# Kernel optimization log

Measured on AMD Instinct MI355X. Metric: run time of the kernel, lower is better.

Reference implementation:

```python
import jax, jax.numpy as jnp
import numpy as np

NEG_SLOPE = 0.2  # PyG GATConv default negative_slope


def gat_conv(x, src, dst, W, a_src, a_dst, bias, concat=True):
    """PyG-style GATConv (self-loops already appended to src/dst).
    x: [N, Fin], W: [Fin, H*C], a_src/a_dst: [H, C], bias: [H*C] or [C].
    """
    N = x.shape[0]
    H, C = a_src.shape
    h = (x @ W).reshape(N, H, C)                       # [N, H, C]
    s_src = jnp.einsum('nhc,hc->nh', h, a_src)         # per-node src logit
    s_dst = jnp.einsum('nhc,hc->nh', h, a_dst)         # per-node dst logit
    e = jax.nn.leaky_relu(s_src[src] + s_dst[dst], NEG_SLOPE)   # [E, H]
    # segment softmax over incoming edges of each destination node
    m = jax.ops.segment_max(e, dst, num_segments=N)    # [N, H]
    ex = jnp.exp(e - m[dst])
    denom = jax.ops.segment_sum(ex, dst, num_segments=N)
    alpha = ex / (denom[dst] + 1e-16)                  # [E, H]
    out = jax.ops.segment_sum(h[src] * alpha[:, :, None], dst, num_segments=N)  # [N,H,C]
    out = out.reshape(N, H * C) if concat else out.mean(axis=1)
    return out + bias


def setup_inputs() -> dict:
    key = jax.random.key(0)
    ks = jax.random.split(key, 12)
    N, E = 20000, 320000
    Fin, Hd, Hh = 384, 256, 4
    x = jax.random.normal(ks[0], (N, Fin), dtype=jnp.float32)
    edge_index = jax.random.randint(ks[1], (2, E), 0, N, dtype=jnp.int32)
    s = lambda k, shp, fan: jax.random.normal(k, shp, dtype=jnp.float32) / np.sqrt(fan)
    return {
        'x': x, 'edge_index': edge_index,
        'W1': s(ks[2], (Fin, Hh * Hd), Fin),
        'a_src1': s(ks[3], (Hh, Hd), Hd), 'a_dst1': s(ks[4], (Hh, Hd), Hd),
        'b1': jnp.zeros((Hh * Hd,), jnp.float32),
        'W2': s(ks[5], (Hh * Hd, Hd), Hh * Hd),
        'a_src2': s(ks[6], (1, Hd), Hd), 'a_dst2': s(ks[7], (1, Hd), Hd),
        'b2': jnp.zeros((Hd,), jnp.float32),
        'Wp1': s(ks[8], (Hd, Hd // 2), Hd), 'bp1': jnp.zeros((Hd // 2,), jnp.float32),
        'Wp2': s(ks[9], (Hd // 2, 1), Hd // 2), 'bp2': jnp.zeros((1,), jnp.float32),
    }


def reference(x, edge_index, W1, a_src1, a_dst1, b1, W2, a_src2, a_dst2, b2,
              Wp1, bp1, Wp2, bp2):
    N = x.shape[0]
    loops = jnp.arange(N, dtype=edge_index.dtype)
    src = jnp.concatenate([edge_index[0], loops])  # PyG add_self_loops=True
    dst = jnp.concatenate([edge_index[1], loops])
    h = jax.nn.elu(gat_conv(x, src, dst, W1, a_src1, a_dst1, b1, concat=True))
    h = jax.nn.elu(gat_conv(h, src, dst, W2, a_src2, a_dst2, b2, concat=True))
    graph_features = jnp.mean(h, axis=0, keepdims=True)  # batch=None path
    infl = jax.nn.sigmoid(jax.nn.relu(h @ Wp1 + bp1) @ Wp2 + bp2)
    return h, graph_features, infl
```

## Files before the change

### kernel.cpp

```cpp
#include <hip/hip_runtime.h>

#define NEG_SLOPE 0.2f
#define SM_SHIFT 3.0f

typedef __bf16 bf16x8 __attribute__((ext_vector_type(8)));
typedef float floatx4 __attribute__((ext_vector_type(4)));
typedef float floatx2 __attribute__((ext_vector_type(2)));
typedef unsigned short ushortx4 __attribute__((ext_vector_type(4)));
typedef unsigned short ushortx8 __attribute__((ext_vector_type(8)));

__device__ __forceinline__ float eluf(float x) { return x > 0.f ? x : __expf(x) - 1.f; }
__device__ __forceinline__ float lrelu(float x) { return x > 0.f ? x : NEG_SLOPE * x; }

__device__ __forceinline__ unsigned short f2bf(float f) {
    unsigned u = __float_as_uint(f);
    u += 0x7FFFu + ((u >> 16) & 1u);
    return (unsigned short)(u >> 16);
}
__device__ __forceinline__ float bf2f(unsigned short h) {
    return __uint_as_float(((unsigned)h) << 16);
}
__device__ __forceinline__ floatx2 mk2(unsigned u) {
    floatx2 r;
    r.x = __uint_as_float(u << 16);
    r.y = __uint_as_float(u & 0xFFFF0000u);
    return r;
}

__device__ __forceinline__ void async16(const unsigned short* g, unsigned short* l) {
    __builtin_amdgcn_global_load_lds(
        (const __attribute__((address_space(1))) unsigned int*)g,
        (__attribute__((address_space(3))) unsigned int*)l,
        16, 0, 0);
}

__global__ __launch_bounds__(256) void prep_kernel(
        const int* __restrict__ ei, int E, int N, int* __restrict__ counts,
        const float* __restrict__ x, unsigned short* __restrict__ xb,
        const float* __restrict__ W1, unsigned short* __restrict__ w1t,
        const float* __restrict__ W2, unsigned short* __restrict__ w2t,
        const float* __restrict__ Wp1, unsigned short* __restrict__ wp1t,
        const float* __restrict__ as1, const float* __restrict__ ad1, float* __restrict__ U) {
    __shared__ float tile[32][33];
    int b = blockIdx.x;
    int t = threadIdx.x;
    int Et = E + N;
    int nA = (Et + 255) >> 8;
    int nB = (N * 96 + 255) >> 8;
    if (b < nA) {
        int i = b * 256 + t;
        if (i < Et) {
            int d = (i < E) ? ei[E + i] : (i - E);
            atomicAdd(&counts[d], 1);
        }
    } else if (b < nA + nB) {
        int i = (b - nA) * 256 + t;
        if (i < N * 96) {
            float4 v = ((const float4*)x)[i];
            ushortx4 o;
            o[0] = f2bf(v.x); o[1] = f2bf(v.y); o[2] = f2bf(v.z); o[3] = f2bf(v.w);
            *(ushortx4*)(xb + (size_t)i * 4) = o;
        }
    } else if (b < nA + nB + 384) {
        int idx = b - nA - nB;
        int n0 = (idx & 31) * 32, k0 = (idx >> 5) * 32;
        int tx = t & 31, ty = t >> 5;
        #pragma unroll
        for (int i = 0; i < 32; i += 8)
            tile[ty + i][tx] = W1[(size_t)(k0 + ty + i) * 1024 + n0 + tx];
        __syncthreads();
        #pragma unroll
        for (int i = 0; i < 32; i += 8)
            w1t[(size_t)(n0 + ty + i) * 384 + k0 + tx] = f2bf(tile[tx][ty + i]);
    } else if (b < nA + nB + 384 + 256) {
        int idx = b - nA - nB - 384;
        int n0 = (idx & 7) * 32, k0 = (idx >> 3) * 32;
        int tx = t & 31, ty = t >> 5;
        #pragma unroll
        for (int i = 0; i < 32; i += 8)
            tile[ty + i][tx] = W2[(size_t)(k0 + ty + i) * 256 + n0 + tx];
        __syncthreads();
        #pragma unroll
        for (int i = 0; i < 32; i += 8)
            w2t[(size_t)(n0 + ty + i) * 1024 + k0 + tx] = f2bf(tile[tx][ty + i]);
    } else if (b < nA + nB + 384 + 256 + 32) {
        int idx = b - nA - nB - 384 - 256;
        int n0 = (idx & 3) * 32, k0 = (idx >> 2) * 32;
        int tx = t & 31, ty = t >> 5;
        #pragma unroll
        for (int i = 0; i < 32; i += 8)
            tile[ty + i][tx] = Wp1[(size_t)(k0 + ty + i) * 128 + n0 + tx];
        __syncthreads();
        #pragma unroll
        for (int i = 0; i < 32; i += 8)
            wp1t[(size_t)(n0 + ty + i) * 256 + k0 + tx] = f2bf(tile[tx][ty + i]);
    } else {
        int idx = b - nA - nB - 384 - 256 - 32;
        int k = idx * 4 + (t >> 6);
        int lane = t & 63;
        #pragma unroll
        for (int r = 0; r < 8; r++) {
            int h = r & 3;
            const float* a = (r < 4 ? as1 : ad1) + h * 256 + lane * 4;
            const float* w = W1 + (size_t)k * 1024 + h * 256 + lane * 4;
            float4 wv = *(const float4*)w;
            float4 av = *(const float4*)a;
            float p = wv.x * av.x + wv.y * av.y + wv.z * av.z + wv.w * av.w;
            #pragma unroll
            for (int off = 32; off; off >>= 1) p += __shfl_xor(p, off);
            if (lane == 0) U[r * 384 + k] = p;
        }
    }
}

__global__ void scan_kernel(int* __restrict__ counts_cursor, int* __restrict__ row_ptr, int N) {
    __shared__ int s_wsum[16];
    __shared__ int s_carry;
    int t = threadIdx.x;
    int lane = t & 63, wid = t >> 6;
    if (t == 0) { s_carry = 0; row_ptr[0] = 0; }
    __syncthreads();
    for (int start = 0; start < N; start += 1024) {
        int i = start + t;
        int v = (i < N) ? counts_cursor[i] : 0;
        int s = v;
        #pragma unroll
        for (int d = 1; d < 64; d <<= 1) {
            int u = __shfl_up(s, d);
            if (lane >= d) s += u;
        }
        if (lane == 63) s_wsum[wid] = s;
        __syncthreads();
        if (wid == 0) {
            int w = (lane < 16) ? s_wsum[lane] : 0;
            #pragma unroll
            for (int d = 1; d < 16; d <<= 1) {
                int u = __shfl_up(w, d);
                if (lane >= d) w += u;
            }
            if (lane < 16) s_wsum[lane] = w;
        }
        __syncthreads();
        int incl = s + (wid ? s_wsum[wid - 1] : 0) + s_carry;
        if (i < N) { row_ptr[i + 1] = incl; counts_cursor[i] = incl - v; }
        __syncthreads();
        if (t == 0) s_carry += s_wsum[15];
        __syncthreads();
    }
}

__global__ void fill_kernel(const int* __restrict__ ei, int E, int N,
                            int* __restrict__ cursor, int* __restrict__ col) {
    int i = blockIdx.x * blockDim.x + threadIdx.x;
    int Et = E + N;
    if (i >= Et) return;
    int s, d;
    if (i < E) { s = ei[i]; d = ei[E + i]; } else { s = d = i - E; }
    int pos = atomicAdd(&cursor[d], 1);
    col[pos] = s;
}

__global__ void sU_kernel(const unsigned short* __restrict__ xb, const float* __restrict__ U,
                          float* __restrict__ ss1, float* __restrict__ sd1, int N) {
    int wid = (blockIdx.x * blockDim.x + threadIdx.x) >> 6;
    int lane = threadIdx.x & 63;
    if (wid >= N) return;
    int half = lane >> 5, l32 = lane & 31;
    int c0 = l32 * 12;
    const unsigned short* row = xb + (size_t)wid * 384 + c0;
    ushortx8 v8 = *(const ushortx8*)row;
    ushortx4 v4 = *(const ushortx4*)(row + 8);
    float xv[12];
    #pragma unroll
    for (int j = 0; j < 8; j++) xv[j] = bf2f(v8[j]);
    #pragma unroll
    for (int j = 0; j < 4; j++) xv[8 + j] = bf2f(v4[j]);
    float p[4];
    #pragma unroll
    for (int r = 0; r < 4; r++) {
        const float* u = U + (half * 4 + r) * 384 + c0;
        float s = 0.f;
        #pragma unroll
        for (int j = 0; j < 12; j++) s += xv[j] * u[j];
        #pragma unroll
        for (int off = 16; off; off >>= 1) s += __shfl_xor(s, off);
        p[r] = s;
    }
    if (l32 == 0) {
        float* dst = half ? (sd1 + wid * 4) : (ss1 + wid * 4);
        dst[0] = p[0]; dst[1] = p[1]; dst[2] = p[2]; dst[3] = p[3];
    }
}

__global__ void s2_kernel(const unsigned short* __restrict__ h2b, const float* __restrict__ a_src,
                          const float* __restrict__ a_dst, float* __restrict__ ssrc,
                          float* __restrict__ sdst, int N) {
    int wid = (blockIdx.x * blockDim.x + threadIdx.x) >> 6;
    int lane = threadIdx.x & 63;
    if (wid >= N) return;
    ushortx4 v = *(const ushortx4*)(h2b + (size_t)wid * 256 + lane * 4);
    float4 a = ((const float4*)a_src)[lane];
    float4 d = ((const float4*)a_dst)[lane];
    float v0 = bf2f(v[0]), v1 = bf2f(v[1]), v2 = bf2f(v[2]), v3 = bf2f(v[3]);
    float s = v0 * a.x + v1 * a.y + v2 * a.z + v3 * a.w;
    float t = v0 * d.x + v1 * d.y + v2 * d.z + v3 * d.w;
    for (int off = 32; off; off >>= 1) { s += __shfl_xor(s, off); t += __shfl_xor(t, off); }
    if (lane == 0) { ssrc[wid] = s; sdst[wid] = t; }
}

__global__ __launch_bounds__(256) void aggx_kernel(const unsigned short* __restrict__ xb,
        const float* __restrict__ ss1, const float* __restrict__ sd1,
        const int* __restrict__ row_ptr, const int* __restrict__ col,
        unsigned short* __restrict__ aggxn, int N) {
    __shared__ unsigned short lds[4][1536];
    __shared__ float pipe[4][72][8];
    int t = threadIdx.x;
    int wv = t >> 6;
    int wid = blockIdx.x * 4 + wv;
    int lane = t & 63;
    bool active = wid < N;
    int half = lane >> 5, l32 = lane & 31;
    int c0 = l32 * 12;
    float4 dsum = {0.f, 0.f, 0.f, 0.f};
    floatx2 acc2[4][6] = {};
    if (active) {
        if (lane < 8) {
            float* pz = &pipe[wv][64 + lane][0];
            #pragma unroll
            for (int j = 0; j < 8; j++) pz[j] = 0.f;
        }
        int base = row_ptr[wid];
        int deg = row_ptr[wid + 1] - base;
        float4 sd = *(const float4*)(sd1 + (size_t)wid * 4);
        for (int chunk = 0; chunk < deg; chunk += 64) {
            int cnt = min(64, deg - chunk);
            int cl = chunk + lane;
            int myO = 0;
            float4 myW = {0.f, 0.f, 0.f, 0.f};
            if (cl < deg) {
                int s = col[base + cl];
                float4 sp = *(const float4*)(ss1 + (size_t)s * 4);
                myW.x = __expf(lrelu(sp.x + sd.x) - SM_SHIFT); dsum.x += myW.x;
                myW.y = __expf(lrelu(sp.y + sd.y) - SM_SHIFT); dsum.y += myW.y;
                myW.z = __expf(lrelu(sp.z + sd.z) - SM_SHIFT); dsum.z += myW.z;
                myW.w = __expf(lrelu(sp.w + sd.w) - SM_SHIFT); dsum.w += myW.w;
                myO = s * 384;
            }
            float* pe = &pipe[wv][lane][0];
            *(float4*)pe = myW;
            pe[4] = __int_as_float(myO);
            int K = (cnt + 1) >> 1;
#define LOADSTG(wS, u4_, u2_, stg) { \
            const float* pq = &pipe[wv][(stg) * 2 + half][0]; \
            wS = *(const float4*)pq; \
            int oN = __float_as_int(pq[4]); \
            const unsigned short* rN = xb + (unsigned)(oN + c0); \
            u4_ = *(const uint4*)rN; u2_ = *(const uint2*)(rN + 8); }
#define CONSUME(cw, u4_, u2_) { \
            floatx2 xv[6]; \
            xv[0] = mk2(u4_.x); xv[1] = mk2(u4_.y); xv[2] = mk2(u4_.z); \
            xv[3] = mk2(u4_.w); xv[4] = mk2(u2_.x); xv[5] = mk2(u2_.y); \
            _Pragma("unroll") for (int j2 = 0; j2 < 6; j2++) { \
                acc2[0][j2] += cw.x * xv[j2]; \
                acc2[1][j2] += cw.y * xv[j2]; \
                acc2[2][j2] += cw.z * xv[j2]; \
                acc2[3][j2] += cw.w * xv[j2]; } }
            float4 wA, wB, wC, wD;
            uint4 uA4, uB4, uC4, uD4;
            uint2 uA2, uB2, uC2, uD2;
            LOADSTG(wA, uA4, uA2, 0)
            LOADSTG(wB, uB4, uB2, 1)
            LOADSTG(wC, uC4, uC2, 2)
            LOADSTG(wD, uD4, uD2, 3)
            int k = 0;
            for (; k + 4 <= K; k += 4) {
                { float4 cw = wA; uint4 u4 = uA4; uint2 u2 = uA2;
                  LOADSTG(wA, uA4, uA2, k + 4) CONSUME(cw, u4, u2) }
                { float4 cw = wB; uint4 u4 = uB4; uint2 u2 = uB2;
                  LOADSTG(wB, uB4, uB2, k + 5) CONSUME(cw, u4, u2) }
                { float4 cw = wC; uint4 u4 = uC4; uint2 u2 = uC2;
                  LOADSTG(wC, uC4, uC2, k + 6) CONSUME(cw, u4, u2) }
                { float4 cw = wD; uint4 u4 = uD4; uint2 u2 = uD2;
                  LOADSTG(wD, uD4, uD2, k + 7) CONSUME(cw, u4, u2) }
            }
            if (k < K)     { CONSUME(wA, uA4, uA2) }
            if (k + 1 < K) { CONSUME(wB, uB4, uB2) }
            if (k + 2 < K) { CONSUME(wC, uC4, uC2) }
#undef LOADSTG
#undef CONSUME
        }
        #pragma unroll
        for (int off = 32; off; off >>= 1) {
            dsum.x += __shfl_xor(dsum.x, off);
            dsum.y += __shfl_xor(dsum.y, off);
            dsum.z += __shfl_xor(dsum.z, off);
            dsum.w += __shfl_xor(dsum.w, off);
        }
        #pragma unroll
        for (int h = 0; h < 4; h++)
            #pragma unroll
            for (int j2 = 0; j2 < 6; j2++) {
                acc2[h][j2].x += __shfl_xor(acc2[h][j2].x, 32);
                acc2[h][j2].y += __shfl_xor(acc2[h][j2].y, 32);
            }
        float dsel0 = half ? dsum.z : dsum.x;
        float dsel1 = half ? dsum.w : dsum.y;
        #pragma unroll
        for (int hh = 0; hh < 2; hh++) {
            int h = half * 2 + hh;
            float dh = hh ? dsel1 : dsel0;
            float inv = 1.f / (dh + 1e-16f);
            ushortx8 o8; ushortx4 o4;
            #pragma unroll
            for (int j = 0; j < 8; j++) {
                float v = half ? acc2[2 + hh][j >> 1][j & 1] : acc2[hh][j >> 1][j & 1];
                o8[j] = f2bf(v * inv);
            }
            #pragma unroll
            for (int j = 0; j < 4; j++) {
                int jj = 8 + j;
                float v = half ? acc2[2 + hh][jj >> 1][jj & 1] : acc2[hh][jj >> 1][jj & 1];
                o4[j] = f2bf(v * inv);
            }
            unsigned short* lp = &lds[wv][h * 384 + c0];
            *(ushortx8*)lp = o8;
            *(ushortx4*)(lp + 8) = o4;
        }
    }
    __syncthreads();
    size_t blockBase = (size_t)blockIdx.x * 4 * 1536;
    const unsigned short* lflat = &lds[0][0];
    #pragma unroll
    for (int j = 0; j < 3; j++) {
        int so = j * 2048 + t * 8;
        int node = blockIdx.x * 4 + so / 1536;
        if (node < N)
            *(ushortx8*)(aggxn + blockBase + so) = *(const ushortx8*)(lflat + so);
    }
}

#define LDK 40

__global__ __launch_bounds__(256) void gemm_l1(const unsigned short* __restrict__ A,
        const unsigned short* __restrict__ Bt, const float* __restrict__ bias,
        unsigned short* __restrict__ Cout, int M) {
    __shared__ unsigned short As[2][128 * 32];
    __shared__ unsigned short Bs[2][128 * 32];
    int t = threadIdx.x;
    int lane = t & 63, wave = t >> 6;
    int wm = (wave >> 1) * 64, wn = (wave & 1) * 64;
    int q = lane >> 4, l16 = lane & 15;
    int row0 = blockIdx.y * 128, col0 = blockIdx.x * 128;
    int hoff = (col0 >> 8) * 384;
    floatx4 acc[4][4] = {};
    int srow = t >> 2, skc = (t & 3) * 8;
    const unsigned short* Ag0 = A + (size_t)min(row0 + srow, M - 1) * 1536 + hoff + skc;
    const unsigned short* Ag1 = A + (size_t)min(row0 + srow + 64, M - 1) * 1536 + hoff + skc;
    const unsigned short* Bg0 = Bt + (size_t)(col0 + srow) * 384 + skc;
    const unsigned short* Bg1 = Bt + (size_t)(col0 + srow + 64) * 384 + skc;
#define STG_L1(buf, kt) \
    async16(Ag0 + (kt), &As[buf][t * 8]); \
    async16(Ag1 + (kt), &As[buf][2048 + t * 8]); \
    async16(Bg0 + (kt), &Bs[buf][t * 8]); \
    async16(Bg1 + (kt), &Bs[buf][2048 + t * 8]);
    STG_L1(0, 0)
    __syncthreads();
    #pragma unroll
    for (int ti = 0; ti < 12; ++ti) {
        int cur = ti & 1;
        if (ti < 11) { STG_L1(cur ^ 1, (ti + 1) * 32) }
        __builtin_amdgcn_sched_barrier(0);
        bf16x8 af[4], bfr[4];
        #pragma unroll
        for (int i = 0; i < 4; i++)
            af[i] = *(const bf16x8*)&As[cur][(wm + i * 16 + l16) * 32 + q * 8];
        #pragma unroll
        for (int j = 0; j < 4; j++)
            bfr[j] = *(const bf16x8*)&Bs[cur][(wn + j * 16 + l16) * 32 + q * 8];
        #pragma unroll
        for (int i = 0; i < 4; i++)
            #pragma unroll
            for (int j = 0; j < 4; j++)
                acc[i][j] = __builtin_amdgcn_mfma_f32_16x16x32_bf16(af[i], bfr[j], acc[i][j], 0, 0, 0);
        __syncthreads();
    }
#undef STG_L1
    float bj[4];
    #pragma unroll
    for (int j = 0; j < 4; j++) bj[j] = bias[col0 + wn + l16 + j * 16];
    #pragma unroll
    for (int i = 0; i < 4; i++) {
        #pragma unroll
        for (int r = 0; r < 4; r++) {
            int grow = row0 + wm + i * 16 + q * 4 + r;
            if (grow < M) {
                unsigned short* cp = Cout + (size_t)grow * 1024 + col0 + wn + l16;
                #pragma unroll
                for (int j = 0; j < 4; j++) cp[j * 16] = f2bf(eluf(acc[i][j][r] + bj[j]));
            }
        }
    }
}

__global__ __launch_bounds__(256) void gemm_l2(const unsigned short* __restrict__ A,
        const unsigned short* __restrict__ Bt, unsigned short* __restrict__ Cout, int M) {
    __shared__ unsigned short As[2][128 * 32];
    __shared__ unsigned short Bs[2][64 * 32];
    int t = threadIdx.x;
    int lane = t & 63, wave = t >> 6;
    int wm = (wave >> 1) * 64, wn = (wave & 1) * 32;
    int q = lane >> 4, l16 = lane & 15;
    int row0 = blockIdx.y * 128, col0 = blockIdx.x * 64;
    floatx4 acc[4][2] = {};
    int srow = t >> 2, skc = (t & 3) * 8;
    const unsigned short* Ag0 = A + (size_t)min(row0 + srow, M - 1) * 1024 + skc;
    const unsigned short* Ag1 = A + (size_t)min(row0 + srow + 64, M - 1) * 1024 + skc;
    const unsigned short* Bg0 = Bt + (size_t)(col0 + srow) * 1024 + skc;
#define STG_L2(buf, kt) \
    async16(Ag0 + (kt), &As[buf][t * 8]); \
    async16(Ag1 + (kt), &As[buf][2048 + t * 8]); \
    async16(Bg0 + (kt), &Bs[buf][t * 8]);
    STG_L2(0, 0)
    __syncthreads();
    #pragma unroll
    for (int ti = 0; ti < 32; ++ti) {
        int cur = ti & 1;
        if (ti < 31) { STG_L2(cur ^ 1, (ti + 1) * 32) }
        __builtin_amdgcn_sched_barrier(0);
        bf16x8 af[4], bfr[2];
        #pragma unroll
        for (int i = 0; i < 4; i++)
            af[i] = *(const bf16x8*)&As[cur][(wm + i * 16 + l16) * 32 + q * 8];
        #pragma unroll
        for (int j = 0; j < 2; j++)
            bfr[j] = *(const bf16x8*)&Bs[cur][(wn + j * 16 + l16) * 32 + q * 8];
        #pragma unroll
        for (int i = 0; i < 4; i++)
            #pragma unroll
            for (int j = 0; j < 2; j++)
                acc[i][j] = __builtin_amdgcn_mfma_f32_16x16x32_bf16(af[i], bfr[j], acc[i][j], 0, 0, 0);
        __syncthreads();
    }
#undef STG_L2
    #pragma unroll
    for (int i = 0; i < 4; i++) {
        #pragma unroll
        for (int r = 0; r < 4; r++) {
            int grow = row0 + wm + i * 16 + q * 4 + r;
            if (grow < M) {
                unsigned short* cp = Cout + (size_t)grow * 256 + col0 + wn + l16;
                #pragma unroll
                for (int j = 0; j < 2; j++) cp[j * 16] = f2bf(acc[i][j][r]);
            }
        }
    }
}

__global__ __launch_bounds__(256) void agg2_kernel(const unsigned short* __restrict__ h2b,
        const float* __restrict__ ss2, const float* __restrict__ sd2,
        const int* __restrict__ row_ptr, const int* __restrict__ col,
        const float* __restrict__ bias, float* __restrict__ out,
        unsigned short* __restrict__ outb, int N) {
    __shared__ float pipe2[4][72][2];
    int t = threadIdx.x;
    int wv = t >> 6;
    int wid = (blockIdx.x * blockDim.x + t) >> 6;
    int lane = t & 63;
    if (wid >= N) return;
    if (lane < 8) {
        pipe2[wv][64 + lane][0] = 0.f;
        pipe2[wv][64 + lane][1] = 0.f;
    }
    int base = row_ptr[wid];
    int deg = row_ptr[wid + 1] - base;
    float sd = sd2[wid];
    floatx2 accA = {0.f, 0.f}, accB = {0.f, 0.f};
    float dsum = 0.f;
    int ch = lane * 4;
    for (int chunk = 0; chunk < deg; chunk += 64) {
        int cnt = min(64, deg - chunk);
        int cl = chunk + lane;
        int myO = 0;
        float myW = 0.f;
        if (cl < deg) {
            int s = col[base + cl];
            myW = __expf(lrelu(ss2[s] + sd) - SM_SHIFT);
            dsum += myW;
            myO = s * 256;
        }
        pipe2[wv][lane][0] = myW;
        pipe2[wv][lane][1] = __int_as_float(myO);
        int K = (cnt + 1) >> 1;
#define LOADSTG2(w0_, w1_, u0_, u1_, stg) { \
        const float* q0 = &pipe2[wv][(stg) * 2][0]; \
        const float* q1 = &pipe2[wv][(stg) * 2 + 1][0]; \
        w0_ = q0[0]; int o0 = __float_as_int(q0[1]); \
        w1_ = q1[0]; int o1 = __float_as_int(q1[1]); \
        u0_ = *(const uint2*)(h2b + (unsigned)(o0 + ch)); \
        u1_ = *(const uint2*)(h2b + (unsigned)(o1 + ch)); }
#define CONSUME2(w0_, w1_, u0_, u1_) { \
        accA += w0_ * mk2(u0_.x); accA += w1_ * mk2(u1_.x); \
        accB += w0_ * mk2(u0_.y); accB += w1_ * mk2(u1_.y); }
        float wa0, wa1, wb0, wb1, wc0, wc1, wd0, wd1;
        uint2 ua0, ua1, ub0, ub1, uc0, uc1, ud0, ud1;
        LOADSTG2(wa0, wa1, ua0, ua1, 0)
        LOADSTG2(wb0, wb1, ub0, ub1, 1)
        LOADSTG2(wc0, wc1, uc0, uc1, 2)
        LOADSTG2(wd0, wd1, ud0, ud1, 3)
        int k = 0;
        for (; k + 4 <= K; k += 4) {
            { float p0 = wa0, p1 = wa1; uint2 v0 = ua0, v1 = ua1;
              LOADSTG2(wa0, wa1, ua0, ua1, k + 4) CONSUME2(p0, p1, v0, v1) }
            { float p0 = wb0, p1 = wb1; uint2 v0 = ub0, v1 = ub1;
              LOADSTG2(wb0, wb1, ub0, ub1, k + 5) CONSUME2(p0, p1, v0, v1) }
            { float p0 = wc0, p1 = wc1; uint2 v0 = uc0, v1 = uc1;
              LOADSTG2(wc0, wc1, uc0, uc1, k + 6) CONSUME2(p0, p1, v0, v1) }
            { float p0 = wd0, p1 = wd1; uint2 v0 = ud0, v1 = ud1;
              LOADSTG2(wd0, wd1, ud0, ud1, k + 7) CONSUME2(p0, p1, v0, v1) }
        }
        if (k < K)     { CONSUME2(wa0, wa1, ua0, ua1) }
        if (k + 1 < K) { CONSUME2(wb0, wb1, ub0, ub1) }
        if (k + 2 < K) { CONSUME2(wc0, wc1, uc0, uc1) }
#undef LOADSTG2
#undef CONSUME2
    }
    #pragma unroll
    for (int off = 32; off; off >>= 1) dsum += __shfl_xor(dsum, off);
    float inv = 1.f / (dsum + 1e-16f);
    float4 o;
    o.x = eluf(accA.x * inv + bias[ch + 0]);
    o.y = eluf(accA.y * inv + bias[ch + 1]);
    o.z = eluf(accB.x * inv + bias[ch + 2]);
    o.w = eluf(accB.y * inv + bias[ch + 3]);
    *(float4*)(out + (size_t)wid * 256 + ch) = o;
    ushortx4 ob;
    ob[0] = f2bf(o.x); ob[1] = f2bf(o.y); ob[2] = f2bf(o.z); ob[3] = f2bf(o.w);
    *(ushortx4*)(outb + (size_t)wid * 256 + ch) = ob;
}

__global__ __launch_bounds__(256) void tail_kernel(const float* __restrict__ h,
        const unsigned short* __restrict__ hbf, const unsigned short* __restrict__ wp1t,
        const float* __restrict__ bp1, const float* __restrict__ Wp2,
        const float* __restrict__ bp2, float* __restrict__ gf, float* __restrict__ infl, int M) {
    int b = blockIdx.x;
    int nInfl = (M + 127) / 128;
    if (b < nInfl) {
        __shared__ unsigned short As[128 * LDK];
        __shared__ unsigned short Bs[128 * LDK];
        __shared__ float partial[2][128];
        int t = threadIdx.x;
        int lane = t & 63, wave = t >> 6;
        int wm = (wave >> 1) * 64, wn = (wave & 1) * 64;
        int q = lane >> 4, l16 = lane & 15;
        int row0 = b * 128;
        floatx4 acc[4][4] = {};
        int sg = (t & 7) * 4;
        int sr = t >> 3;
        for (int kt = 0; kt < 256; kt += 32) {
            #pragma unroll
            for (int p = 0; p < 4; p++) {
                int r = sr + p * 32;
                int ga = min(row0 + r, M - 1);
                *(ushortx4*)&As[r * LDK + sg] = *(const ushortx4*)(hbf + (size_t)ga * 256 + kt + sg);
                *(ushortx4*)&Bs[r * LDK + sg] = *(const ushortx4*)(wp1t + (size_t)r * 256 + kt + sg);
            }
            __syncthreads();
            bf16x8 af[4], bfr[4];
            #pragma unroll
            for (int i = 0; i < 4; i++)
                af[i] = *(const bf16x8*)&As[(wm + i * 16 + l16) * LDK + q * 8];
            #pragma unroll
            for (int j = 0; j < 4; j++)
                bfr[j] = *(const bf16x8*)&Bs[(wn + j * 16 + l16) * LDK + q * 8];
            #pragma unroll
            for (int i = 0; i < 4; i++)
                #pragma unroll
                for (int j = 0; j < 4; j++)
                    acc[i][j] = __builtin_amdgcn_mfma_f32_16x16x32_bf16(af[i], bfr[j], acc[i][j], 0, 0, 0);
            __syncthreads();
        }
        float b1v[4], w2v[4];
        #pragma unroll
        for (int j = 0; j < 4; j++) {
            int colj = wn + j * 16 + l16;
            b1v[j] = bp1[colj];
            w2v[j] = Wp2[colj];
        }
        #pragma unroll
        for (int i = 0; i < 4; i++) {
            #pragma unroll
            for (int r = 0; r < 4; r++) {
                float s = fmaxf(acc[i][0][r] + b1v[0], 0.f) * w2v[0]
                        + fmaxf(acc[i][1][r] + b1v[1], 0.f) * w2v[1]
                        + fmaxf(acc[i][2][r] + b1v[2], 0.f) * w2v[2]
                        + fmaxf(acc[i][3][r] + b1v[3], 0.f) * w2v[3];
                #pragma unroll
                for (int off = 1; off < 16; off <<= 1) s += __shfl_xor(s, off);
                if (l16 == 0) partial[wave & 1][wm + i * 16 + q * 4 + r] = s;
            }
        }
        __syncthreads();
        if (t < 128) {
            int row = row0 + t;
            if (row < M) {
                float v = partial[0][t] + partial[1][t] + bp2[0];
                infl[row] = 1.f / (1.f + __expf(-v));
            }
        }
    } else {
        int bb = b - nInfl;
        int c = threadIdx.x;
        int per = (M + 159) / 160;
        int n0 = bb * per;
        int n1 = min(M, n0 + per);
        float a0 = 0.f, a1 = 0.f, a2 = 0.f, a3 = 0.f;
        float a4 = 0.f, a5 = 0.f, a6 = 0.f, a7 = 0.f;
        int n = n0;
        for (; n + 8 <= n1; n += 8) {
            a0 += h[(size_t)(n + 0) * 256 + c];
            a1 += h[(size_t)(n + 1) * 256 + c];
            a2 += h[(size_t)(n + 2) * 256 + c];
            a3 += h[(size_t)(n + 3) * 256 + c];
            a4 += h[(size_t)(n + 4) * 256 + c];
            a5 += h[(size_t)(n + 5) * 256 + c];
            a6 += h[(size_t)(n + 6) * 256 + c];
            a7 += h[(size_t)(n + 7) * 256 + c];
        }
        for (; n < n1; n++) a0 += h[(size_t)n * 256 + c];
        float acc = ((a0 + a1) + (a2 + a3)) + ((a4 + a5) + (a6 + a7));
        atomicAdd(&gf[c], acc * (1.0f / M));
    }
}

extern "C" void kernel_launch(void* const* d_in, const int* in_sizes, int n_in,
                              void* d_out, int out_size, void* d_ws, size_t ws_size,
                              hipStream_t stream) {
    const float* x   = (const float*)d_in[0];
    const int*   ei  = (const int*)d_in[1];
    const float* W1  = (const float*)d_in[2];
    const float* as1 = (const float*)d_in[3];
    const float* ad1 = (const float*)d_in[4];
    const float* b1  = (const float*)d_in[5];
    const float* W2  = (const float*)d_in[6];
    const float* as2 = (const float*)d_in[7];
    const float* ad2 = (const float*)d_in[8];
    const float* b2  = (const float*)d_in[9];
    const float* Wp1 = (const float*)d_in[10];
    const float* bp1 = (const float*)d_in[11];
    const float* Wp2 = (const float*)d_in[12];
    const float* bp2 = (const float*)d_in[13];

    const int N  = in_sizes[0] / 384;
    const int E  = in_sizes[1] / 2;
    const int Et = E + N;

    char* wsp = (char*)d_ws;
    unsigned short* xb    = (unsigned short*)wsp; wsp += (size_t)N * 384  * sizeof(short);
    unsigned short* aggxn = (unsigned short*)wsp; wsp += (size_t)N * 1536 * sizeof(short);
    unsigned short* h1eb  = (unsigned short*)wsp; wsp += (size_t)N * 1024 * sizeof(short);
    unsigned short* h2b   = (unsigned short*)wsp; wsp += (size_t)N * 256  * sizeof(short);
    unsigned short* hbf   = (unsigned short*)wsp; wsp += (size_t)N * 256  * sizeof(short);
    unsigned short* w1t   = (unsigned short*)wsp; wsp += (size_t)1024 * 384 * sizeof(short);
    unsigned short* w2t   = (unsigned short*)wsp; wsp += (size_t)256 * 1024 * sizeof(short);
    unsigned short* wp1t  = (unsigned short*)wsp; wsp += (size_t)128 * 256 * sizeof(short);
    float* U   = (float*)wsp; wsp += (size_t)8 * 384 * sizeof(float);
    float* ss1 = (float*)wsp; wsp += (size_t)N * 4 * sizeof(float);
    float* sd1 = (float*)wsp; wsp += (size_t)N * 4 * sizeof(float);
    float* ss2 = (float*)wsp; wsp += (size_t)N * sizeof(float);
    float* sd2 = (float*)wsp; wsp += (size_t)N * sizeof(float);
    int* row_ptr = (int*)wsp; wsp += (size_t)(N + 1) * sizeof(int);
    int* cursor  = (int*)wsp; wsp += (size_t)N * sizeof(int);
    int* col     = (int*)wsp;

    float* out_h  = (float*)d_out;
    float* out_gf = out_h + (size_t)N * 256;
    float* out_if = out_gf + 256;

    hipMemsetAsync(cursor, 0, (size_t)N * sizeof(int), stream);
    int nA = (Et + 255) / 256;
    int nB = (N * 96 + 255) / 256;
    int nPrep = nA + nB + 384 + 256 + 32 + 96;
    prep_kernel<<<nPrep, 256, 0, stream>>>(ei, E, N, cursor, x, xb, W1, w1t, W2, w2t, Wp1, wp1t, as1, ad1, U);
    scan_kernel<<<1, 1024, 0, stream>>>(cursor, row_ptr, N);
    fill_kernel<<<nA, 256, 0, stream>>>(ei, E, N, cursor, col);

    sU_kernel<<<(N + 3) / 4, 256, 0, stream>>>(xb, U, ss1, sd1, N);
    aggx_kernel<<<(N + 3) / 4, 256, 0, stream>>>(xb, ss1, sd1, row_ptr, col, aggxn, N);
    gemm_l1<<<dim3(8, (N + 127) / 128), 256, 0, stream>>>(aggxn, w1t, b1, h1eb, N);

    gemm_l2<<<dim3(4, (N + 127) / 128), 256, 0, stream>>>(h1eb, w2t, h2b, N);
    s2_kernel<<<(N + 3) / 4, 256, 0, stream>>>(h2b, as2, ad2, ss2, sd2, N);
    agg2_kernel<<<(N + 3) / 4, 256, 0, stream>>>(h2b, ss2, sd2, row_ptr, col, b2, out_h, hbf, N);

    hipMemsetAsync(out_gf, 0, 256 * sizeof(float), stream);
    tail_kernel<<<(N + 127) / 128 + 160, 256, 0, stream>>>(out_h, hbf, wp1t, bp1, Wp2, bp2, out_gf, out_if, N);
}
```

Measured before the change: 334.7 us.

## Split layer-1 aggregation across two waves per node and deepen layer-2 gather pipeline

The layer-1 neighbor aggregation now assigns two wavefronts per destination node, each covering half of the 384 feature columns. This halves per-thread accumulators and load width, which lowers register pressure and raises the number of independent gathers in flight. The cost is that each wave recomputes the per-edge softmax weights, so that work is duplicated. Separately, the layer-2 aggregation's software pipeline is deepened from 4 to 6 stages, with the padded LDS region enlarged to match, to hide more gather latency at the cost of more registers.

```diff
diff --git a/kernel.cpp b/kernel.cpp
--- a/kernel.cpp
+++ b/kernel.cpp
@@ -212,17 +212,19 @@
         const float* __restrict__ ss1, const float* __restrict__ sd1,
         const int* __restrict__ row_ptr, const int* __restrict__ col,
         unsigned short* __restrict__ aggxn, int N) {
-    __shared__ unsigned short lds[4][1536];
+    __shared__ unsigned short ldso[2][1536];
     __shared__ float pipe[4][72][8];
     int t = threadIdx.x;
     int wv = t >> 6;
-    int wid = blockIdx.x * 4 + wv;
+    int nl = wv >> 1;
+    int hw = wv & 1;
+    int wid = blockIdx.x * 2 + nl;
     int lane = t & 63;
+    int half = lane >> 5, l32 = lane & 31;
+    int c0 = hw * 192 + l32 * 6;
     bool active = wid < N;
-    int half = lane >> 5, l32 = lane & 31;
-    int c0 = l32 * 12;
     float4 dsum = {0.f, 0.f, 0.f, 0.f};
-    floatx2 acc2[4][6] = {};
+    floatx2 acc2[4][3] = {};
     if (active) {
         if (lane < 8) {
             float* pz = &pipe[wv][64 + lane][0];
@@ -250,42 +252,38 @@
             *(float4*)pe = myW;
             pe[4] = __int_as_float(myO);
             int K = (cnt + 1) >> 1;
-#define LOADSTG(wS, u4_, u2_, stg) { \
+#define LOADSTG(wS, a_, b_, c_, stg) { \
             const float* pq = &pipe[wv][(stg) * 2 + half][0]; \
             wS = *(const float4*)pq; \
             int oN = __float_as_int(pq[4]); \
-            const unsigned short* rN = xb + (unsigned)(oN + c0); \
-            u4_ = *(const uint4*)rN; u2_ = *(const uint2*)(rN + 8); }
-#define CONSUME(cw, u4_, u2_) { \
-            floatx2 xv[6]; \
-            xv[0] = mk2(u4_.x); xv[1] = mk2(u4_.y); xv[2] = mk2(u4_.z); \
-            xv[3] = mk2(u4_.w); xv[4] = mk2(u2_.x); xv[5] = mk2(u2_.y); \
-            _Pragma("unroll") for (int j2 = 0; j2 < 6; j2++) { \
-                acc2[0][j2] += cw.x * xv[j2]; \
-                acc2[1][j2] += cw.y * xv[j2]; \
-                acc2[2][j2] += cw.z * xv[j2]; \
-                acc2[3][j2] += cw.w * xv[j2]; } }
+            const unsigned* rN = (const unsigned*)(xb + (unsigned)(oN + c0)); \
+            a_ = rN[0]; b_ = rN[1]; c_ = rN[2]; }
+#define CONSUME(cw, a_, b_, c_) { \
+            floatx2 xv0 = mk2(a_), xv1 = mk2(b_), xv2 = mk2(c_); \
+            acc2[0][0] += cw.x * xv0; acc2[0][1] += cw.x * xv1; acc2[0][2] += cw.x * xv2; \
+            acc2[1][0] += cw.y * xv0; acc2[1][1] += cw.y * xv1; acc2[1][2] += cw.y * xv2; \
+            acc2[2][0] += cw.z * xv0; acc2[2][1] += cw.z * xv1; acc2[2][2] += cw.z * xv2; \
+            acc2[3][0] += cw.w * xv0; acc2[3][1] += cw.w * xv1; acc2[3][2] += cw.w * xv2; }
             float4 wA, wB, wC, wD;
-            uint4 uA4, uB4, uC4, uD4;
-            uint2 uA2, uB2, uC2, uD2;
-            LOADSTG(wA, uA4, uA2, 0)
-            LOADSTG(wB, uB4, uB2, 1)
-            LOADSTG(wC, uC4, uC2, 2)
-            LOADSTG(wD, uD4, uD2, 3)
+            unsigned aA, bA, cA, aB, bB, cB, aC, bC, cC, aD, bD, cD;
+            LOADSTG(wA, aA, bA, cA, 0)
+            LOADSTG(wB, aB, bB, cB, 1)
+            LOADSTG(wC, aC, bC, cC, 2)
+            LOADSTG(wD, aD, bD, cD, 3)
             int k = 0;
             for (; k + 4 <= K; k += 4) {
-                { float4 cw = wA; uint4 u4 = uA4; uint2 u2 = uA2;
-                  LOADSTG(wA, uA4, uA2, k + 4) CONSUME(cw, u4, u2) }
-                { float4 cw = wB; uint4 u4 = uB4; uint2 u2 = uB2;
-                  LOADSTG(wB, uB4, uB2, k + 5) CONSUME(cw, u4, u2) }
-                { float4 cw = wC; uint4 u4 = uC4; uint2 u2 = uC2;
-                  LOADSTG(wC, uC4, uC2, k + 6) CONSUME(cw, u4, u2) }
-                { float4 cw = wD; uint4 u4 = uD4; uint2 u2 = uD2;
-                  LOADSTG(wD, uD4, uD2, k + 7) CONSUME(cw, u4, u2) }
-            }
-            if (k < K)     { CONSUME(wA, uA4, uA2) }
-            if (k + 1 < K) { CONSUME(wB, uB4, uB2) }
-            if (k + 2 < K) { CONSUME(wC, uC4, uC2) }
+                { float4 cw = wA; unsigned a_ = aA, b_ = bA, c_ = cA;
+                  LOADSTG(wA, aA, bA, cA, k + 4) CONSUME(cw, a_, b_, c_) }
+                { float4 cw = wB; unsigned a_ = aB, b_ = bB, c_ = cB;
+                  LOADSTG(wB, aB, bB, cB, k + 5) CONSUME(cw, a_, b_, c_) }
+                { float4 cw = wC; unsigned a_ = aC, b_ = bC, c_ = cC;
+                  LOADSTG(wC, aC, bC, cC, k + 6) CONSUME(cw, a_, b_, c_) }
+                { float4 cw = wD; unsigned a_ = aD, b_ = bD, c_ = cD;
+                  LOADSTG(wD, aD, bD, cD, k + 7) CONSUME(cw, a_, b_, c_) }
+            }
+            if (k < K)     { CONSUME(wA, aA, bA, cA) }
+            if (k + 1 < K) { CONSUME(wB, aB, bB, cB) }
+            if (k + 2 < K) { CONSUME(wC, aC, bC, cC) }
 #undef LOADSTG
 #undef CONSUME
         }
@@ -299,43 +297,41 @@
         #pragma unroll
         for (int h = 0; h < 4; h++)
             #pragma unroll
-            for (int j2 = 0; j2 < 6; j2++) {
+            for (int j2 = 0; j2 < 3; j2++) {
                 acc2[h][j2].x += __shfl_xor(acc2[h][j2].x, 32);
                 acc2[h][j2].y += __shfl_xor(acc2[h][j2].y, 32);
             }
-        float dsel0 = half ? dsum.z : dsum.x;
-        float dsel1 = half ? dsum.w : dsum.y;
-        #pragma unroll
-        for (int hh = 0; hh < 2; hh++) {
-            int h = half * 2 + hh;
-            float dh = hh ? dsel1 : dsel0;
-            float inv = 1.f / (dh + 1e-16f);
-            ushortx8 o8; ushortx4 o4;
-            #pragma unroll
-            for (int j = 0; j < 8; j++) {
-                float v = half ? acc2[2 + hh][j >> 1][j & 1] : acc2[hh][j >> 1][j & 1];
-                o8[j] = f2bf(v * inv);
-            }
-            #pragma unroll
-            for (int j = 0; j < 4; j++) {
-                int jj = 8 + j;
-                float v = half ? acc2[2 + hh][jj >> 1][jj & 1] : acc2[hh][jj >> 1][jj & 1];
-                o4[j] = f2bf(v * inv);
-            }
-            unsigned short* lp = &lds[wv][h * 384 + c0];
-            *(ushortx8*)lp = o8;
-            *(ushortx4*)(lp + 8) = o4;
+        float invh[4];
+        invh[0] = 1.f / (dsum.x + 1e-16f);
+        invh[1] = 1.f / (dsum.y + 1e-16f);
+        invh[2] = 1.f / (dsum.z + 1e-16f);
+        invh[3] = 1.f / (dsum.w + 1e-16f);
+        if (half == 0) {
+            unsigned short* lp0 = &ldso[nl][c0];
+            #pragma unroll
+            for (int h = 0; h < 4; h++) {
+                float iv = invh[h];
+                unsigned* dst = (unsigned*)(lp0 + h * 384);
+                #pragma unroll
+                for (int p = 0; p < 3; p++) {
+                    unsigned lo = f2bf(acc2[h][p].x * iv);
+                    unsigned hi = f2bf(acc2[h][p].y * iv);
+                    dst[p] = lo | (hi << 16);
+                }
+            }
         }
     }
     __syncthreads();
-    size_t blockBase = (size_t)blockIdx.x * 4 * 1536;
-    const unsigned short* lflat = &lds[0][0];
-    #pragma unroll
-    for (int j = 0; j < 3; j++) {
+    size_t blockBase = (size_t)blockIdx.x * 2 * 1536;
+    const unsigned short* lflat = &ldso[0][0];
+    #pragma unroll
+    for (int j = 0; j < 2; j++) {
         int so = j * 2048 + t * 8;
-        int node = blockIdx.x * 4 + so / 1536;
-        if (node < N)
-            *(ushortx8*)(aggxn + blockBase + so) = *(const ushortx8*)(lflat + so);
+        if (so < 3072) {
+            int node = blockIdx.x * 2 + so / 1536;
+            if (node < N)
+                *(ushortx8*)(aggxn + blockBase + so) = *(const ushortx8*)(lflat + so);
+        }
     }
 }
 
@@ -461,13 +457,13 @@
         const int* __restrict__ row_ptr, const int* __restrict__ col,
         const float* __restrict__ bias, float* __restrict__ out,
         unsigned short* __restrict__ outb, int N) {
-    __shared__ float pipe2[4][72][2];
+    __shared__ float pipe2[4][76][2];
     int t = threadIdx.x;
     int wv = t >> 6;
     int wid = (blockIdx.x * blockDim.x + t) >> 6;
     int lane = t & 63;
     if (wid >= N) return;
-    if (lane < 8) {
+    if (lane < 12) {
         pipe2[wv][64 + lane][0] = 0.f;
         pipe2[wv][64 + lane][1] = 0.f;
     }
@@ -501,26 +497,34 @@
 #define CONSUME2(w0_, w1_, u0_, u1_) { \
         accA += w0_ * mk2(u0_.x); accA += w1_ * mk2(u1_.x); \
         accB += w0_ * mk2(u0_.y); accB += w1_ * mk2(u1_.y); }
-        float wa0, wa1, wb0, wb1, wc0, wc1, wd0, wd1;
-        uint2 ua0, ua1, ub0, ub1, uc0, uc1, ud0, ud1;
+        float wa0, wa1, wb0, wb1, wc0, wc1, wd0, wd1, we0, we1, wf0, wf1;
+        uint2 ua0, ua1, ub0, ub1, uc0, uc1, ud0, ud1, ue0, ue1, uf0, uf1;
         LOADSTG2(wa0, wa1, ua0, ua1, 0)
         LOADSTG2(wb0, wb1, ub0, ub1, 1)
         LOADSTG2(wc0, wc1, uc0, uc1, 2)
         LOADSTG2(wd0, wd1, ud0, ud1, 3)
+        LOADSTG2(we0, we1, ue0, ue1, 4)
+        LOADSTG2(wf0, wf1, uf0, uf1, 5)
         int k = 0;
-        for (; k + 4 <= K; k += 4) {
+        for (; k + 6 <= K; k += 6) {
             { float p0 = wa0, p1 = wa1; uint2 v0 = ua0, v1 = ua1;
-              LOADSTG2(wa0, wa1, ua0, ua1, k + 4) CONSUME2(p0, p1, v0, v1) }
+              LOADSTG2(wa0, wa1, ua0, ua1, k + 6) CONSUME2(p0, p1, v0, v1) }
             { float p0 = wb0, p1 = wb1; uint2 v0 = ub0, v1 = ub1;
-              LOADSTG2(wb0, wb1, ub0, ub1, k + 5) CONSUME2(p0, p1, v0, v1) }
+              LOADSTG2(wb0, wb1, ub0, ub1, k + 7) CONSUME2(p0, p1, v0, v1) }
             { float p0 = wc0, p1 = wc1; uint2 v0 = uc0, v1 = uc1;
-              LOADSTG2(wc0, wc1, uc0, uc1, k + 6) CONSUME2(p0, p1, v0, v1) }
+              LOADSTG2(wc0, wc1, uc0, uc1, k + 8) CONSUME2(p0, p1, v0, v1) }
             { float p0 = wd0, p1 = wd1; uint2 v0 = ud0, v1 = ud1;
-              LOADSTG2(wd0, wd1, ud0, ud1, k + 7) CONSUME2(p0, p1, v0, v1) }
+              LOADSTG2(wd0, wd1, ud0, ud1, k + 9) CONSUME2(p0, p1, v0, v1) }
+            { float p0 = we0, p1 = we1; uint2 v0 = ue0, v1 = ue1;
+              LOADSTG2(we0, we1, ue0, ue1, k + 10) CONSUME2(p0, p1, v0, v1) }
+            { float p0 = wf0, p1 = wf1; uint2 v0 = uf0, v1 = uf1;
+              LOADSTG2(wf0, wf1, uf0, uf1, k + 11) CONSUME2(p0, p1, v0, v1) }
         }
         if (k < K)     { CONSUME2(wa0, wa1, ua0, ua1) }
         if (k + 1 < K) { CONSUME2(wb0, wb1, ub0, ub1) }
         if (k + 2 < K) { CONSUME2(wc0, wc1, uc0, uc1) }
+        if (k + 3 < K) { CONSUME2(wd0, wd1, ud0, ud1) }
+        if (k + 4 < K) { CONSUME2(we0, we1, ue0, ue1) }
 #undef LOADSTG2
 #undef CONSUME2
     }
@@ -685,7 +689,7 @@
     fill_kernel<<<nA, 256, 0, stream>>>(ei, E, N, cursor, col);
 
     sU_kernel<<<(N + 3) / 4, 256, 0, stream>>>(xb, U, ss1, sd1, N);
-    aggx_kernel<<<(N + 3) / 4, 256, 0, stream>>>(xb, ss1, sd1, row_ptr, col, aggxn, N);
+    aggx_kernel<<<(N + 1) / 2, 256, 0, stream>>>(xb, ss1, sd1, row_ptr, col, aggxn, N);
     gemm_l1<<<dim3(8, (N + 127) / 128), 256, 0, stream>>>(aggxn, w1t, b1, h1eb, N);
 
     gemm_l2<<<dim3(4, (N + 127) / 128), 256, 0, stream>>>(h1eb, w2t, h2b, N);
```

New measurement: 341.4 us. +2.0%, slower.
